# Kernel tuning notes

Hardware: AMD Instinct MI355X
Metric: run time of the kernel (lower is better)

## Reference

```python
import jax, jax.numpy as jnp
import numpy as np

N, F, H = 512, 256, 512

def _w(k, i, o):
    return jax.random.normal(k, (i, o), jnp.float32) * (1.0 / np.sqrt(i))

def setup_inputs() -> dict:
    key = jax.random.key(0)
    ks = jax.random.split(key, 12)
    z = lambda n: jnp.zeros((n,), jnp.float32)
    return {
        "node_features": jax.random.normal(ks[0], (N, F), jnp.float32),
        "adjacency": jax.random.uniform(ks[1], (N, N), jnp.float32),
        # GraphConv layers: neighbor linear (wl,bl) and self-loop (ws,bs)
        "gc1_wl": _w(ks[2], F, H), "gc1_bl": z(H), "gc1_ws": _w(ks[3], F, H), "gc1_bs": z(H),
        "gc2_wl": _w(ks[4], H, H), "gc2_bl": z(H), "gc2_ws": _w(ks[5], H, H), "gc2_bs": z(H),
        "gc3_wl": _w(ks[6], H, F), "gc3_bl": z(F), "gc3_ws": _w(ks[7], H, F), "gc3_bs": z(F),
        # edge MLP: Linear(2F,H) -> ReLU -> (dropout=identity, eval) -> Linear(H,H) -> ReLU -> Linear(H,1)
        "mlp_w1": _w(ks[8], 2 * F, H), "mlp_b1": z(H),
        "mlp_w2": _w(ks[9], H, H), "mlp_b2": z(H),
        "mlp_w3": _w(ks[10], H, 1), "mlp_b3": z(1),
    }

def _gconv(x, adj_norm, wl, bl, ws, bs):
    # adj_norm @ Linear(x) + SelfLoop(x)
    return adj_norm @ (x @ wl + bl) + (x @ ws + bs)

def reference(node_features, adjacency,
              gc1_wl, gc1_bl, gc1_ws, gc1_bs,
              gc2_wl, gc2_bl, gc2_ws, gc2_bs,
              gc3_wl, gc3_bl, gc3_ws, gc3_bs,
              mlp_w1, mlp_b1, mlp_w2, mlp_b2, mlp_w3, mlp_b3):
    # row-normalized adjacency (shared across all three layers)
    adj_norm = adjacency / (adjacency.sum(axis=1, keepdims=True) + 1e-8)
    x = jax.nn.relu(_gconv(node_features, adj_norm, gc1_wl, gc1_bl, gc1_ws, gc1_bs))
    x = jax.nn.relu(_gconv(x, adj_norm, gc2_wl, gc2_bl, gc2_ws, gc2_bs))
    emb = _gconv(x, adj_norm, gc3_wl, gc3_bl, gc3_ws, gc3_bs)  # [N, F]
    # vectorized all-pairs (i<j) edge scoring, symmetric scatter
    iu, ju = np.triu_indices(N, k=1)  # static index lists, P = N(N-1)/2
    ef = jnp.concatenate([emb[iu], emb[ju]], axis=-1)  # [P, 2F]
    h = jax.nn.relu(ef @ mlp_w1 + mlp_b1)
    h = jax.nn.relu(h @ mlp_w2 + mlp_b2)
    s = jax.nn.sigmoid((h @ mlp_w3 + mlp_b3)[:, 0])  # [P]
    edge_scores = jnp.zeros((N, N), emb.dtype).at[iu, ju].set(s).at[ju, iu].set(s)
    return emb, edge_scores
```

## Files before the change

### kernel.cpp

```cpp
#include <hip/hip_runtime.h>
#include <hip/hip_bf16.h>


#define NN 512
#define FF 256
#define HH 512

typedef __attribute__((ext_vector_type(8))) short s8v;
typedef __attribute__((ext_vector_type(4))) float f4v;

__device__ __forceinline__ ushort f2bf(float f) {
  unsigned u = __float_as_uint(f);
  unsigned r = (u + 0x7fffu + ((u >> 16) & 1u)) >> 16;
  return (ushort)r;
}

template <bool RELU>
__device__ __forceinline__ void gemm_tile64(
    int m0, int n0, int K,
    const float* __restrict__ A, int lda,
    const float* __restrict__ B, int ldb,
    const float* __restrict__ bias,
    const float* __restrict__ add, int ldadd,
    float* __restrict__ C, int ldc, int tid)
{
  __shared__ float As[64][18];
  __shared__ float Bs[64][68];
  float4 acc = {0.f, 0.f, 0.f, 0.f};
  const int ty = tid >> 4, tx = tid & 15;

  const int am = tid >> 4;
  const int ak = tid & 15;
  const int bk = tid >> 4;
  const int bn = tid & 15;

  float4 pa = *(const float4*)&A[(m0 + am) * lda + ak * 4];
  float4 pb0 = *(const float4*)&B[bk * ldb + n0 + bn * 4];
  float4 pb1 = *(const float4*)&B[(bk + 16) * ldb + n0 + bn * 4];
  float4 pb2 = *(const float4*)&B[(bk + 32) * ldb + n0 + bn * 4];
  float4 pb3 = *(const float4*)&B[(bk + 48) * ldb + n0 + bn * 4];

  for (int k0 = 0; k0 < K; k0 += 64) {
    As[ak * 4 + 0][am] = pa.x;
    As[ak * 4 + 1][am] = pa.y;
    As[ak * 4 + 2][am] = pa.z;
    As[ak * 4 + 3][am] = pa.w;
    *(float4*)&Bs[bk][bn * 4] = pb0;
    *(float4*)&Bs[bk + 16][bn * 4] = pb1;
    *(float4*)&Bs[bk + 32][bn * 4] = pb2;
    *(float4*)&Bs[bk + 48][bn * 4] = pb3;
    __syncthreads();
    if (k0 + 64 < K) {
      pa = *(const float4*)&A[(m0 + am) * lda + k0 + 64 + ak * 4];
      pb0 = *(const float4*)&B[(k0 + 64 + bk) * ldb + n0 + bn * 4];
      pb1 = *(const float4*)&B[(k0 + 80 + bk) * ldb + n0 + bn * 4];
      pb2 = *(const float4*)&B[(k0 + 96 + bk) * ldb + n0 + bn * 4];
      pb3 = *(const float4*)&B[(k0 + 112 + bk) * ldb + n0 + bn * 4];
    }
#pragma unroll
    for (int k = 0; k < 64; ++k) {
      float a = As[k][ty];
      float4 b = *(const float4*)&Bs[k][tx * 4];
      acc.x += a * b.x; acc.y += a * b.y; acc.z += a * b.z; acc.w += a * b.w;
    }
    __syncthreads();
  }

  int m = m0 + ty;
  float4 v = acc;
  if (bias) {
    float4 bv = *(const float4*)&bias[n0 + tx * 4];
    v.x += bv.x; v.y += bv.y; v.z += bv.z; v.w += bv.w;
  }
  if (add) {
    float4 d = *(const float4*)&add[m * ldadd + n0 + tx * 4];
    v.x += d.x; v.y += d.y; v.z += d.z; v.w += d.w;
  }
  if (RELU) {
    v.x = fmaxf(v.x, 0.f); v.y = fmaxf(v.y, 0.f);
    v.z = fmaxf(v.z, 0.f); v.w = fmaxf(v.w, 0.f);
  }
  *(float4*)&C[m * ldc + n0 + tx * 4] = v;
}

__global__ __launch_bounds__(256)
void prep_gemm1(const float* __restrict__ adj, float* __restrict__ adjn,
                const float* __restrict__ w2, ushort* __restrict__ w2t2,
                const float* __restrict__ node,
                const float* __restrict__ g1wl, const float* __restrict__ g1bl,
                const float* __restrict__ g1ws, const float* __restrict__ g1bs,
                float* __restrict__ Tb, float* __restrict__ Sb) {
  int b = blockIdx.x;
  int tid = threadIdx.x;
  if (b < 512) {
    int z = b >> 8, t = b & 255;
    int m0 = (t >> 3) * 16, n0 = (t & 7) * 64;
    gemm_tile64<false>(m0, n0, FF, node, FF, z ? g1ws : g1wl, HH,
                       z ? g1bs : g1bl, nullptr, 0, z ? Sb : Tb, HH, tid);
  } else if (b < 1024) {
    int row = b - 512;
    const float* r = adj + row * NN;
    float a0 = r[tid], a1 = r[tid + 256];
    float s = a0 + a1;
#pragma unroll
    for (int m = 1; m < 64; m <<= 1) s += __shfl_xor(s, m);
    __shared__ float wsum[4];
    if ((tid & 63) == 0) wsum[tid >> 6] = s;
    __syncthreads();
    float inv = 1.f / (wsum[0] + wsum[1] + wsum[2] + wsum[3] + 1e-8f);
    float* o = adjn + row * NN;
    o[tid] = a0 * inv;
    o[tid + 256] = a1 * inv;
  } else {
    int b2 = b - 1024;
    int slab = b2 >> 3;
    int col = (b2 & 7) * 64 + (tid >> 2);
    int kq = tid & 3;
    int k0 = slab * 32 + kq * 8;
    ushort tmp[8];
#pragma unroll
    for (int e = 0; e < 8; ++e) tmp[e] = f2bf(w2[(k0 + e) * HH + col]);
    ushort* dst = w2t2 + slab * 16384 + col * 32 + kq * 8;
    *(ushort4*)dst = *(ushort4*)tmp;
    *(ushort4*)(dst + 4) = *(ushort4*)&tmp[4];
  }
}

template <bool RELU>
__global__ __launch_bounds__(256)
void gemm_ts(int K,
             const float* __restrict__ A, int lda,
             const float* __restrict__ B0, const float* __restrict__ B1, int ldb,
             const float* __restrict__ bias0, const float* __restrict__ bias1,
             const float* __restrict__ add0, const float* __restrict__ add1, int ldadd,
             float* __restrict__ C0, float* __restrict__ C1, int ldc)
{
  const float* B = blockIdx.z ? B1 : B0;
  const float* bias = blockIdx.z ? bias1 : bias0;
  const float* add = blockIdx.z ? add1 : add0;
  float* C = blockIdx.z ? C1 : C0;
  gemm_tile64<RELU>(blockIdx.y * 16, blockIdx.x * 64, K, A, lda, B, ldb,
                    bias, add, ldadd, C, ldc, threadIdx.x);
}

__global__ __launch_bounds__(512)
__attribute__((amdgpu_waves_per_eu(2, 2)))
void edge_mlp(const float* __restrict__ Amat, const float* __restrict__ Bmat,
              const ushort* __restrict__ w2t2,
              const float* __restrict__ b2, const float* __restrict__ w3,
              const float* __restrict__ b3,
              float* __restrict__ edges)
{
  __shared__ ushort h1s[2][128 * 128];
  __shared__ float rowsv[2][24][128];
  __shared__ float part[8][128];

  const int tb = (int)blockIdx.x;
  int bj = (int)((sqrtf(4.f * tb + 1.f) - 1.f) * 0.5f);
  while (bj * bj + bj > tb) --bj;
  while ((bj + 1) * (bj + 2) <= tb) ++bj;
  const int bi = tb - bj * bj - bj;

  const int tid = threadIdx.x;
  const int wid = tid >> 6;
  const int lane = tid & 63;
  const int l15 = lane & 15;
  const int lg = lane >> 4;

  const f4v zero = {0.f, 0.f, 0.f, 0.f};
  f4v acc[8][4];
#pragma unroll
  for (int mf = 0; mf < 8; ++mf)
#pragma unroll
    for (int nf = 0; nf < 4; ++nf) acc[mf][nf] = zero;

  const int r1 = tid >> 5, kc1 = tid & 31;
  const int r2 = 16 + (tid >> 5);
  const float* src1base = (r1 < 8) ? (Amat + (bi * 8 + r1) * HH)
                                   : (Bmat + (bj * 16 + r1 - 8) * HH);
  const float* src2base = Bmat + (bj * 16 + r2 - 8) * HH;

  float4 ra, rb;
  auto issue_rows = [&](int ch) {
    ra = *(const float4*)(src1base + ch * 128 + kc1 * 4);
    if (tid < 256) rb = *(const float4*)(src2base + ch * 128 + kc1 * 4);
  };
  auto write_rows = [&](int buf) {
    *(float4*)&rowsv[buf][r1][kc1 * 4] = ra;
    if (tid < 256) *(float4*)&rowsv[buf][r2][kc1 * 4] = rb;
  };
  auto build_h1 = [&](int buf) {
#pragma unroll
    for (int q = 0; q < 8; ++q) {
      int fidx = q * 512 + tid;
      int p = fidx >> 5;
      int k4 = fidx & 31;
      float4 av = *(const float4*)&rowsv[buf][p >> 4][k4 * 4];
      float4 bv = *(const float4*)&rowsv[buf][8 + (p & 15)][k4 * 4];
      ushort4 pk;
      pk.x = f2bf(fmaxf(av.x + bv.x, 0.f));
      pk.y = f2bf(fmaxf(av.y + bv.y, 0.f));
      pk.z = f2bf(fmaxf(av.z + bv.z, 0.f));
      pk.w = f2bf(fmaxf(av.w + bv.w, 0.f));
      int off = (p * 256 + k4 * 8) ^ ((p & 7) << 4);
      *(ushort4*)((char*)h1s[buf] + off) = pk;
    }
  };

  auto lgkm_barrier = [] {
    asm volatile("s_waitcnt lgkmcnt(0)" ::: "memory");
    __builtin_amdgcn_s_barrier();
  };

  issue_rows(0);
  write_rows(0);
  lgkm_barrier();
  build_h1(0);
  lgkm_barrier();

  const ushort* wbase = w2t2 + wid * 2048 + l15 * 32 + lg * 8;

  s8v nb0, nb1, nb2, nb3;
  nb0 = *(const s8v*)wbase;
  nb1 = *(const s8v*)(wbase + 512);
  nb2 = *(const s8v*)(wbase + 1024);
  nb3 = *(const s8v*)(wbase + 1536);

  auto slab_step = [&](int cur, int slab) {
    s8v cb0 = nb0, cb1 = nb1, cb2 = nb2, cb3 = nb3;
    if (slab < 15) {
      const ushort* wb = wbase + (slab + 1) * 16384;
      nb0 = *(const s8v*)wb;
      nb1 = *(const s8v*)(wb + 512);
      nb2 = *(const s8v*)(wb + 1024);
      nb3 = *(const s8v*)(wb + 1536);
    }
    int ks = slab & 3;
    __builtin_amdgcn_s_setprio(1);
#pragma unroll
    for (int mf = 0; mf < 8; ++mf) {
      int p = mf * 16 + l15;
      int off = (p * 256 + ks * 64 + lg * 16) ^ ((p & 7) << 4);
      s8v a = *(const s8v*)((const char*)h1s[cur] + off);
      acc[mf][0] = __builtin_amdgcn_mfma_f32_16x16x32_bf16(a, cb0, acc[mf][0], 0, 0, 0);
      acc[mf][1] = __builtin_amdgcn_mfma_f32_16x16x32_bf16(a, cb1, acc[mf][1], 0, 0, 0);
      acc[mf][2] = __builtin_amdgcn_mfma_f32_16x16x32_bf16(a, cb2, acc[mf][2], 0, 0, 0);
      acc[mf][3] = __builtin_amdgcn_mfma_f32_16x16x32_bf16(a, cb3, acc[mf][3], 0, 0, 0);
    }
    __builtin_amdgcn_s_setprio(0);
  };

#pragma unroll
  for (int ch = 0; ch < 4; ++ch) {
    int cur = ch & 1;
    if (ch < 3) issue_rows(ch + 1);
    slab_step(cur, ch * 4 + 0);
    slab_step(cur, ch * 4 + 1);
    if (ch < 3) write_rows(cur ^ 1);
    slab_step(cur, ch * 4 + 2);
    if (ch < 3) lgkm_barrier();
    slab_step(cur, ch * 4 + 3);
    if (ch < 3) {
      build_h1(cur ^ 1);
      lgkm_barrier();
    }
  }

  float bb[4], ww[4];
#pragma unroll
  for (int nf = 0; nf < 4; ++nf) {
    int col = wid * 64 + nf * 16 + l15;
    bb[nf] = b2[col];
    ww[nf] = w3[col];
  }
#pragma unroll
  for (int mf = 0; mf < 8; ++mf) {
    float ps[4];
#pragma unroll
    for (int e = 0; e < 4; ++e) {
      ps[e] = fmaxf(acc[mf][0][e] + bb[0], 0.f) * ww[0] +
              fmaxf(acc[mf][1][e] + bb[1], 0.f) * ww[1] +
              fmaxf(acc[mf][2][e] + bb[2], 0.f) * ww[2] +
              fmaxf(acc[mf][3][e] + bb[3], 0.f) * ww[3];
    }
#pragma unroll
    for (int m = 1; m < 16; m <<= 1) {
#pragma unroll
      for (int e = 0; e < 4; ++e) ps[e] += __shfl_xor(ps[e], m);
    }
    if (l15 == 0) {
#pragma unroll
      for (int e = 0; e < 4; ++e)
        part[wid][mf * 16 + lg * 4 + e] = ps[e];
    }
  }
  __syncthreads();
  if (tid < 128) {
    float tot = b3[0];
#pragma unroll
    for (int w = 0; w < 8; ++w) tot += part[w][tid];
    float sg = 1.f / (1.f + expf(-tot));
    int i = bi * 8 + (tid >> 4);
    int j = bj * 16 + (tid & 15);
    if (i < j) {
      edges[i * NN + j] = sg;
      edges[j * NN + i] = sg;
    } else if (i == j) {
      edges[i * NN + i] = 0.f;
    }
  }
}

extern "C" void kernel_launch(void* const* d_in, const int* in_sizes, int n_in,
                              void* d_out, int out_size, void* d_ws, size_t ws_size,
                              hipStream_t stream) {
  const float* node = (const float*)d_in[0];
  const float* adj  = (const float*)d_in[1];
  const float* g1wl = (const float*)d_in[2];
  const float* g1bl = (const float*)d_in[3];
  const float* g1ws = (const float*)d_in[4];
  const float* g1bs = (const float*)d_in[5];
  const float* g2wl = (const float*)d_in[6];
  const float* g2bl = (const float*)d_in[7];
  const float* g2ws = (const float*)d_in[8];
  const float* g2bs = (const float*)d_in[9];
  const float* g3wl = (const float*)d_in[10];
  const float* g3bl = (const float*)d_in[11];
  const float* g3ws = (const float*)d_in[12];
  const float* g3bs = (const float*)d_in[13];
  const float* w1 = (const float*)d_in[14];
  const float* b1 = (const float*)d_in[15];
  const float* w2 = (const float*)d_in[16];
  const float* b2 = (const float*)d_in[17];
  const float* w3 = (const float*)d_in[18];
  const float* b3 = (const float*)d_in[19];

  float* out = (float*)d_out;
  float* emb = out;
  float* edges = out + NN * FF;

  char* wsb = (char*)d_ws;
  float* adjn = (float*)wsb;
  float* Tb   = (float*)(wsb + (1u << 20));
  float* Sb   = (float*)(wsb + (2u << 20));
  float* xa   = (float*)(wsb + (3u << 20));
  float* xb   = (float*)(wsb + (4u << 20));
  ushort* w2t2 = (ushort*)(wsb + (5u << 20));
  float* Amat = Tb;
  float* Bmat = Sb;

  prep_gemm1<<<1152, 256, 0, stream>>>(adj, adjn, w2, w2t2, node,
                                       g1wl, g1bl, g1ws, g1bs, Tb, Sb);
  gemm_ts<true><<<dim3(8, 32, 1), 256, 0, stream>>>(
      NN, adjn, NN, Tb, Tb, HH, nullptr, nullptr,
      Sb, Sb, HH, xa, xa, HH);
  gemm_ts<false><<<dim3(8, 32, 2), 256, 0, stream>>>(
      HH, xa, HH, g2wl, g2ws, HH, g2bl, g2bs,
      nullptr, nullptr, 0, Tb, Sb, HH);
  gemm_ts<true><<<dim3(8, 32, 1), 256, 0, stream>>>(
      NN, adjn, NN, Tb, Tb, HH, nullptr, nullptr,
      Sb, Sb, HH, xb, xb, HH);
  gemm_ts<false><<<dim3(4, 32, 2), 256, 0, stream>>>(
      HH, xb, HH, g3wl, g3ws, FF, g3bl, g3bs,
      nullptr, nullptr, 0, Tb, Sb, FF);
  gemm_ts<false><<<dim3(4, 32, 1), 256, 0, stream>>>(
      NN, adjn, NN, Tb, Tb, FF, nullptr, nullptr,
      Sb, Sb, FF, emb, emb, FF);
  gemm_ts<false><<<dim3(8, 32, 2), 256, 0, stream>>>(
      FF, emb, FF, w1, w1 + FF * HH, HH, b1, nullptr,
      nullptr, nullptr, 0, Amat, Bmat, HH);

  edge_mlp<<<1056, 512, 0, stream>>>(Amat, Bmat, w2t2, b2, w3, b3, edges);
}
```

Before: 180.0 us.

## Use 8-row adjacency GEMM kernel with register prefetch for propagation layers

Adds a dedicated gemm_adj8 kernel for the three adjacency-propagation GEMMs. It uses 8x64 output tiles, which doubles the block count to fill more compute units, and prefetches the next K-slice into registers while the current slice is computed from shared memory. The cost it targets is low occupancy and exposed load latency in the small 512x512 GEMMs. In exchange each thread computes only two outputs, which lowers arithmetic intensity and increases B-tile reloads.

```diff
diff --git a/kernel.cpp b/kernel.cpp
--- a/kernel.cpp
+++ b/kernel.cpp
@@ -81,6 +81,74 @@
     v.z = fmaxf(v.z, 0.f); v.w = fmaxf(v.w, 0.f);
   }
   *(float4*)&C[m * ldc + n0 + tx * 4] = v;
+}
+
+template <bool RELU>
+__global__ __launch_bounds__(256)
+void gemm_adj8(int K,
+               const float* __restrict__ A, int lda,
+               const float* __restrict__ B, int ldb,
+               const float* __restrict__ add, int ldadd,
+               float* __restrict__ C, int ldc)
+{
+  const int n0 = blockIdx.x * 64;
+  const int m0 = blockIdx.y * 8;
+  const int tid = threadIdx.x;
+  const int ty = tid >> 5;
+  const int tx = tid & 31;
+
+  __shared__ float As[64][9];
+  __shared__ float Bs[64][68];
+  float2 acc = {0.f, 0.f};
+
+  const int ar = tid >> 5;
+  const int ak2 = tid & 31;
+  const int bk = tid >> 4;
+  const int bn = tid & 15;
+
+  float2 pa = *(const float2*)&A[(m0 + ar) * lda + ak2 * 2];
+  float4 pb0 = *(const float4*)&B[bk * ldb + n0 + bn * 4];
+  float4 pb1 = *(const float4*)&B[(bk + 16) * ldb + n0 + bn * 4];
+  float4 pb2 = *(const float4*)&B[(bk + 32) * ldb + n0 + bn * 4];
+  float4 pb3 = *(const float4*)&B[(bk + 48) * ldb + n0 + bn * 4];
+
+  for (int k0 = 0; k0 < K; k0 += 64) {
+    As[ak2 * 2][ar] = pa.x;
+    As[ak2 * 2 + 1][ar] = pa.y;
+    *(float4*)&Bs[bk][bn * 4] = pb0;
+    *(float4*)&Bs[bk + 16][bn * 4] = pb1;
+    *(float4*)&Bs[bk + 32][bn * 4] = pb2;
+    *(float4*)&Bs[bk + 48][bn * 4] = pb3;
+    __syncthreads();
+    if (k0 + 64 < K) {
+      pa = *(const float2*)&A[(m0 + ar) * lda + k0 + 64 + ak2 * 2];
+      pb0 = *(const float4*)&B[(k0 + 64 + bk) * ldb + n0 + bn * 4];
+      pb1 = *(const float4*)&B[(k0 + 80 + bk) * ldb + n0 + bn * 4];
+      pb2 = *(const float4*)&B[(k0 + 96 + bk) * ldb + n0 + bn * 4];
+      pb3 = *(const float4*)&B[(k0 + 112 + bk) * ldb + n0 + bn * 4];
+    }
+#pragma unroll
+    for (int k = 0; k < 64; ++k) {
+      float a = As[k][ty];
+      float2 b = *(const float2*)&Bs[k][tx * 2];
+      acc.x += a * b.x;
+      acc.y += a * b.y;
+    }
+    __syncthreads();
+  }
+
+  int m = m0 + ty;
+  int col = n0 + tx * 2;
+  float2 v = acc;
+  if (add) {
+    float2 d = *(const float2*)&add[m * ldadd + col];
+    v.x += d.x; v.y += d.y;
+  }
+  if (RELU) {
+    v.x = fmaxf(v.x, 0.f);
+    v.y = fmaxf(v.y, 0.f);
+  }
+  *(float2*)&C[m * ldc + col] = v;
 }
 
 __global__ __launch_bounds__(256)
@@ -351,21 +419,18 @@
 
   prep_gemm1<<<1152, 256, 0, stream>>>(adj, adjn, w2, w2t2, node,
                                        g1wl, g1bl, g1ws, g1bs, Tb, Sb);
-  gemm_ts<true><<<dim3(8, 32, 1), 256, 0, stream>>>(
-      NN, adjn, NN, Tb, Tb, HH, nullptr, nullptr,
-      Sb, Sb, HH, xa, xa, HH);
+  gemm_adj8<true><<<dim3(8, 64), 256, 0, stream>>>(
+      NN, adjn, NN, Tb, HH, Sb, HH, xa, HH);
   gemm_ts<false><<<dim3(8, 32, 2), 256, 0, stream>>>(
       HH, xa, HH, g2wl, g2ws, HH, g2bl, g2bs,
       nullptr, nullptr, 0, Tb, Sb, HH);
-  gemm_ts<true><<<dim3(8, 32, 1), 256, 0, stream>>>(
-      NN, adjn, NN, Tb, Tb, HH, nullptr, nullptr,
-      Sb, Sb, HH, xb, xb, HH);
+  gemm_adj8<true><<<dim3(8, 64), 256, 0, stream>>>(
+      NN, adjn, NN, Tb, HH, Sb, HH, xb, HH);
   gemm_ts<false><<<dim3(4, 32, 2), 256, 0, stream>>>(
       HH, xb, HH, g3wl, g3ws, FF, g3bl, g3bs,
       nullptr, nullptr, 0, Tb, Sb, FF);
-  gemm_ts<false><<<dim3(4, 32, 1), 256, 0, stream>>>(
-      NN, adjn, NN, Tb, Tb, FF, nullptr, nullptr,
-      Sb, Sb, FF, emb, emb, FF);
+  gemm_adj8<false><<<dim3(4, 64), 256, 0, stream>>>(
+      NN, adjn, NN, Tb, FF, Sb, FF, emb, FF);
   gemm_ts<false><<<dim3(8, 32, 2), 256, 0, stream>>>(
       FF, emb, FF, w1, w1 + FF * HH, HH, b1, nullptr,
       nullptr, nullptr, 0, Amat, Bmat, HH);
```

New measurement: 184.3 us. +2.4%, slower.
